# Kernel tuning notes

Hardware: AMD Instinct MI355X
Metric: run time of the kernel (lower is better)

Reference implementation:

```python
import jax, jax.numpy as jnp
import numpy as np

B_, S_, DIM, DT_RANK, D_STATE = 4, 1024, 384, 24, 16


def layer_norm(x, g, b, eps=1e-5):
    mu = jnp.mean(x, axis=-1, keepdims=True)
    var = jnp.mean((x - mu) ** 2, axis=-1, keepdims=True)
    return (x - mu) * jax.lax.rsqrt(var + eps) * g + b


def conv1d(x, w, b):
    # x: (B, C, L), w: (O, I, K), 'same' padding for odd K
    pad = (w.shape[-1] - 1) // 2
    y = jax.lax.conv_general_dilated(x, w, (1,), [(pad, pad)],
                                     dimension_numbers=('NCH', 'OIH', 'NCH'))
    return y + b[None, :, None]


def ssm(x, w_dbc, w_dt, b_dt, A_log, D):
    # x: (b, s, d) -> selective scan (Mamba), parallel (associative) scan form
    dbc = jnp.einsum('bsd,ed->bse', x, w_dbc)
    delta, Bm, Cm = jnp.split(dbc, [DT_RANK, DT_RANK + D_STATE], axis=-1)
    delta = jax.nn.softplus(jnp.einsum('bsr,dr->bsd', delta, w_dt) + b_dt)  # (b,s,d)
    A = -jnp.exp(A_log)                                   # (d, n)
    deltaA = jnp.exp(delta[..., None] * A)                # (b,s,d,n)
    BX = (delta * x)[..., None] * Bm[:, :, None, :]       # (b,s,d,n)

    def combine(c1, c2):
        a1, h1 = c1
        a2, h2 = c2
        return a1 * a2, a2 * h1 + h2

    _, hs = jax.lax.associative_scan(combine, (deltaA, BX), axis=1)
    y = jnp.einsum('bsdn,bsn->bsd', hs, Cm)
    return y + D * x


def setup_inputs() -> dict:
    key = jax.random.key(0)
    ks = jax.random.split(key, 16)
    sc = 0.02
    d, r, n = DIM, DT_RANK, D_STATE
    A_log = jnp.log(jnp.tile(jnp.arange(1, n + 1, dtype=jnp.float32), (d, 1)))  # (d, n)
    return {
        'x': jax.random.normal(ks[0], (B_, S_, d), dtype=jnp.float32),
        'w_p1': jax.random.normal(ks[1], (d, d, 3)) * sc, 'b_p1': jnp.zeros((d,)),
        'w_p2': jax.random.normal(ks[2], (d, d, 3)) * sc, 'b_p2': jnp.zeros((d,)),
        'w_p3': jax.random.normal(ks[3], (d, d, 1)) * sc, 'b_p3': jnp.zeros((d,)),
        'w_cf': jax.random.normal(ks[4], (d, d, 1)) * sc, 'b_cf': jnp.zeros((d,)),
        'w_cb': jax.random.normal(ks[5], (d, d, 1)) * sc, 'b_cb': jnp.zeros((d,)),
        'g_n': jnp.ones((d,)), 'bt_n': jnp.zeros((d,)),
        'g_nf': jnp.ones((d,)), 'bt_nf': jnp.zeros((d,)),
        'g_nb': jnp.ones((d,)), 'bt_nb': jnp.zeros((d,)),
        'w_dbc1': jax.random.normal(ks[6], (r + 2 * n, d)) * sc,
        'w_dt1': jax.random.normal(ks[7], (d, r)) * sc, 'b_dt1': jnp.zeros((d,)),
        'A_log1': A_log, 'D1': jnp.ones((d,)),
        'w_dbc2': jax.random.normal(ks[8], (r + 2 * n, d)) * sc,
        'w_dt2': jax.random.normal(ks[9], (d, r)) * sc, 'b_dt2': jnp.zeros((d,)),
        'A_log2': A_log, 'D2': jnp.ones((d,)),
    }


def reference(x, w_p1, b_p1, w_p2, b_p2, w_p3, b_p3, w_cf, b_cf, w_cb, b_cb,
              g_n, bt_n, g_nf, bt_nf, g_nb, bt_nb,
              w_dbc1, w_dt1, b_dt1, A_log1, D1,
              w_dbc2, w_dt2, b_dt2, A_log2, D2):
    skip = x
    xn = layer_norm(x, g_n, bt_n)
    xt = jnp.swapaxes(xn, 1, 2)                       # (b, d, s)
    z1 = jnp.swapaxes(conv1d(xt, w_p1, b_p1), 1, 2)   # (b, s, d)
    xp = conv1d(xt, w_p2, b_p2)                       # (b, d, s)

    def direction(xd, wc, bc, g, bt, w_dbc, w_dt, b_dt, A_log, D):
        h = conv1d(xd, wc, bc)
        h = jnp.swapaxes(h, 1, 2)
        h = layer_norm(h, g, bt)
        return ssm(h, w_dbc, w_dt, b_dt, A_log, D)

    x1 = direction(xp, w_cf, b_cf, g_nf, bt_nf, w_dbc1, w_dt1, b_dt1, A_log1, D1)
    # backward direction: sequence flipped (note: original does NOT flip back)
    x2 = direction(xp[:, :, ::-1], w_cb, b_cb, g_nb, bt_nb, w_dbc2, w_dt2, b_dt2, A_log2, D2)

    z = jax.nn.silu(z1)
    x3 = jnp.swapaxes((x1 + x2) * z, 1, 2)            # (b, d, s)
    out = jnp.swapaxes(conv1d(x3, w_p3, b_p3), 1, 2)
    return out + skip
```

## Files before the change

kernel.cpp:

```cpp
#include <hip/hip_runtime.h>
#include <cstddef>

#define NB 4
#define NS 1024
#define ND 384
#define NN 16
#define MTOT 4096
#define TM 8
#define NCH 32
#define CHL 32

__global__ __launch_bounds__(256) void prep_weights(
    const float* __restrict__ w_p1, const float* __restrict__ w_p2,
    const float* __restrict__ w_p3, const float* __restrict__ w_cf,
    const float* __restrict__ w_cb,
    const float* __restrict__ w_dbc1, const float* __restrict__ w_dbc2,
    const float* __restrict__ w_dt1,  const float* __restrict__ w_dt2,
    float* __restrict__ wp1T, float* __restrict__ wp2T, float* __restrict__ wp3T,
    float* __restrict__ wcfT, float* __restrict__ wcbT,
    float* __restrict__ wdbc1T, float* __restrict__ wdbc2T,
    float* __restrict__ wdt1T,  float* __restrict__ wdt2T)
{
    int idx = blockIdx.x * 256 + threadIdx.x;
    if (idx < 884736) {
        int q = idx; const float* w; float* wT;
        if (q < 442368) { w = w_p1; wT = wp1T; }
        else            { q -= 442368; w = w_p2; wT = wp2T; }
        int o = q % 384; int ki = q / 384; int i = ki % 384; int k = ki / 384;
        wT[q] = w[((size_t)o * 384 + i) * 3 + k];
    } else if (idx < 1327104) {
        int q = idx - 884736; const float* w; float* wT;
        if (q < 147456)      { w = w_p3; wT = wp3T; }
        else if (q < 294912) { q -= 147456; w = w_cf; wT = wcfT; }
        else                 { q -= 294912; w = w_cb; wT = wcbT; }
        int o = q % 384; int i = q / 384;
        wT[q] = w[(size_t)o * 384 + i];
    } else if (idx < 1370112) {
        int q = idx - 1327104; const float* w; float* wT;
        if (q < 21504) { w = w_dbc1; wT = wdbc1T; }
        else           { q -= 21504; w = w_dbc2; wT = wdbc2T; }
        int e = q % 56; int i = q / 56;
        wT[q] = w[(size_t)e * 384 + i];
    } else if (idx < 1388544) {
        int q = idx - 1370112; const float* w; float* wT;
        if (q < 9216) { w = w_dt1; wT = wdt1T; }
        else          { q -= 9216; w = w_dt2; wT = wdt2T; }
        int d = q % 384; int qq = q / 384;
        wT[q] = w[(size_t)d * 24 + qq];
    }
}

__global__ __launch_bounds__(384) void conv3x2(
    const float* __restrict__ x,
    const float* __restrict__ g_n, const float* __restrict__ bt_n,
    const float* __restrict__ wp2T, const float* __restrict__ b_p2,
    const float* __restrict__ wp1T, const float* __restrict__ b_p1,
    float* __restrict__ XP, float* __restrict__ Z1)
{
    __shared__ float xn[TM + 2][ND];
    int m0 = blockIdx.x * TM;
    int b = m0 >> 10, s0 = m0 & 1023;
    int t = threadIdx.x, wid = t >> 6, lane = t & 63;

    for (int j = wid; j < TM + 2; j += 6) {
        int r = s0 - 1 + j;
        if (r < 0 || r >= NS) {
            for (int e = 0; e < 6; ++e) xn[j][lane + 64 * e] = 0.f;
        } else {
            const float* row = x + ((size_t)(b * NS + r)) * ND;
            float v[6]; float s1 = 0.f, s2 = 0.f;
            #pragma unroll
            for (int e = 0; e < 6; ++e) {
                v[e] = row[lane + 64 * e];
                s1 += v[e]; s2 += v[e] * v[e];
            }
            #pragma unroll
            for (int o = 32; o; o >>= 1) {
                s1 += __shfl_xor(s1, o);
                s2 += __shfl_xor(s2, o);
            }
            float mu = s1 * (1.f / ND);
            float var = s2 * (1.f / ND) - mu * mu;
            float rs = rsqrtf(var + 1e-5f);
            #pragma unroll
            for (int e = 0; e < 6; ++e) {
                int i = lane + 64 * e;
                xn[j][i] = (v[e] - mu) * rs * g_n[i] + bt_n[i];
            }
        }
    }
    __syncthreads();

    float a2[TM], a1[TM];
    #pragma unroll
    for (int r = 0; r < TM; ++r) { a2[r] = b_p2[t]; a1[r] = b_p1[t]; }

    for (int k = 0; k < 3; ++k) {
        const float* w2base = wp2T + ((size_t)k * 384) * 384 + t;
        const float* w1base = wp1T + ((size_t)k * 384) * 384 + t;
        for (int i4 = 0; i4 < 96; ++i4) {
            float4 xv[TM];
            #pragma unroll
            for (int r = 0; r < TM; ++r)
                xv[r] = *reinterpret_cast<const float4*>(&xn[k + r][i4 * 4]);
            const float* w2 = w2base + (size_t)(i4 * 4) * 384;
            const float* w1 = w1base + (size_t)(i4 * 4) * 384;
            #pragma unroll
            for (int e = 0; e < 4; ++e) {
                float wv2 = w2[e * 384];
                float wv1 = w1[e * 384];
                #pragma unroll
                for (int r = 0; r < TM; ++r) {
                    float xe = (e == 0 ? xv[r].x : e == 1 ? xv[r].y :
                                e == 2 ? xv[r].z : xv[r].w);
                    a2[r] = fmaf(xe, wv2, a2[r]);
                    a1[r] = fmaf(xe, wv1, a1[r]);
                }
            }
        }
    }
    #pragma unroll
    for (int r = 0; r < TM; ++r) {
        size_t ix = (size_t)(m0 + r) * ND + t;
        XP[ix] = a2[r];
        Z1[ix] = a1[r];
    }
}

__global__ __launch_bounds__(384) void dir_k1(
    const float* __restrict__ XP, int flip,
    const float* __restrict__ wcT, const float* __restrict__ b_c,
    const float* __restrict__ g, const float* __restrict__ bt,
    const float* __restrict__ wdbcT, const float* __restrict__ wdtT,
    const float* __restrict__ b_dt,
    float* __restrict__ LNo, float* __restrict__ DBCo, float* __restrict__ DELo)
{
    __shared__ float xp[TM][ND];
    __shared__ float uo[TM][ND];
    __shared__ float red[TM][6][2];
    __shared__ float dbcS[TM][56];
    int m0 = blockIdx.x * TM;
    int b = m0 >> 10, s0 = m0 & 1023;
    int t = threadIdx.x, wid = t >> 6, lane = t & 63;

    for (int j = wid; j < TM; j += 6) {
        int s = s0 + j;
        int sE = flip ? (NS - 1 - s) : s;
        const float* row = XP + ((size_t)(b * NS + sE)) * ND;
        for (int e = 0; e < 6; ++e) xp[j][lane + 64 * e] = row[lane + 64 * e];
    }
    __syncthreads();

    float acc[TM];
    #pragma unroll
    for (int r = 0; r < TM; ++r) acc[r] = b_c[t];
    for (int i4 = 0; i4 < 96; ++i4) {
        float4 xv[TM];
        #pragma unroll
        for (int r = 0; r < TM; ++r)
            xv[r] = *reinterpret_cast<const float4*>(&xp[r][i4 * 4]);
        const float* wc = wcT + (size_t)(i4 * 4) * 384 + t;
        #pragma unroll
        for (int e = 0; e < 4; ++e) {
            float wv = wc[e * 384];
            #pragma unroll
            for (int r = 0; r < TM; ++r) {
                float xe = (e == 0 ? xv[r].x : e == 1 ? xv[r].y :
                            e == 2 ? xv[r].z : xv[r].w);
                acc[r] = fmaf(xe, wv, acc[r]);
            }
        }
    }

    #pragma unroll
    for (int r = 0; r < TM; ++r) {
        float s1 = acc[r], s2 = acc[r] * acc[r];
        #pragma unroll
        for (int o = 32; o; o >>= 1) {
            s1 += __shfl_xor(s1, o);
            s2 += __shfl_xor(s2, o);
        }
        if (lane == 0) { red[r][wid][0] = s1; red[r][wid][1] = s2; }
    }
    __syncthreads();
    float gt = g[t], btt = bt[t];
    #pragma unroll
    for (int r = 0; r < TM; ++r) {
        float s1 = 0.f, s2 = 0.f;
        #pragma unroll
        for (int w = 0; w < 6; ++w) { s1 += red[r][w][0]; s2 += red[r][w][1]; }
        float mu = s1 * (1.f / ND);
        float var = s2 * (1.f / ND) - mu * mu;
        float rs = rsqrtf(var + 1e-5f);
        float ln = (acc[r] - mu) * rs * gt + btt;
        uo[r][t] = ln;
        LNo[(size_t)(m0 + r) * ND + t] = ln;
    }
    __syncthreads();

    for (int r = wid; r < TM; r += 6) {
        if (lane < 56) {
            float a = 0.f;
            for (int i = 0; i < ND; ++i)
                a = fmaf(uo[r][i], wdbcT[i * 56 + lane], a);
            dbcS[r][lane] = a;
            DBCo[(size_t)(m0 + r) * 56 + lane] = a;
        }
    }
    __syncthreads();

    float accD[TM]; float bd = b_dt[t];
    #pragma unroll
    for (int r = 0; r < TM; ++r) accD[r] = bd;
    for (int q = 0; q < 24; ++q) {
        float wv = wdtT[q * 384 + t];
        #pragma unroll
        for (int r = 0; r < TM; ++r) accD[r] = fmaf(dbcS[r][q], wv, accD[r]);
    }
    #pragma unroll
    for (int r = 0; r < TM; ++r) {
        float a = accD[r];
        DELo[(size_t)(m0 + r) * ND + t] =
            fmaxf(a, 0.f) + log1pf(__expf(-fabsf(a)));
    }
}

__global__ __launch_bounds__(384) void scan_s1(
    const float* __restrict__ DEL2, const float* __restrict__ LN2,
    const float* __restrict__ DBC2, const float* __restrict__ A_log1,
    const float* __restrict__ A_log2,
    float* __restrict__ P, float* __restrict__ H)
{
    __shared__ float bc[CHL][32];
    int blk = blockIdx.x;
    int c = blk & (NCH - 1);
    int db = blk >> 5;
    int dir = db >> 2, b = db & 3;
    int t = threadIdx.x;
    const float* del  = DEL2 + (size_t)dir * MTOT * ND;
    const float* u    = LN2  + (size_t)dir * MTOT * ND;
    const float* dbc  = DBC2 + (size_t)dir * MTOT * 56;
    const float* Alog = dir ? A_log2 : A_log1;

    for (int e = t; e < CHL * 32; e += 384) {
        int row = e >> 5, col = e & 31;
        bc[row][col] = dbc[((size_t)(b * NS + c * CHL + row)) * 56 + 24 + col];
    }
    __syncthreads();

    float A[NN], h[NN], p[NN];
    #pragma unroll
    for (int n = 0; n < NN; ++n) {
        A[n] = -__expf(Alog[(size_t)t * NN + n]);
        h[n] = 0.f; p[n] = 1.f;
    }
    for (int j = 0; j < CHL; ++j) {
        size_t rix = (size_t)b * NS + c * CHL + j;
        float dl = del[rix * ND + t];
        float uv = u[rix * ND + t];
        float dx = dl * uv;
        #pragma unroll
        for (int n = 0; n < NN; ++n) {
            float da = __expf(dl * A[n]);
            h[n] = fmaf(da, h[n], dx * bc[j][n]);
            p[n] *= da;
        }
    }
    size_t base = ((size_t)blk * ND + t) * NN;
    #pragma unroll
    for (int n = 0; n < NN; ++n) { P[base + n] = p[n]; H[base + n] = h[n]; }
}

__global__ __launch_bounds__(256) void scan_s2(
    float* __restrict__ P, const float* __restrict__ H)
{
    int gid = blockIdx.x * 256 + threadIdx.x;
    int n = gid & 15;
    int d = (gid >> 4) % ND;
    int db = gid / (16 * ND);
    float h = 0.f;
    for (int c = 0; c < NCH; ++c) {
        size_t idx = (((size_t)db * NCH + c) * ND + d) * NN + n;
        float p = P[idx];
        float hh = H[idx];
        P[idx] = h;
        h = fmaf(p, h, hh);
    }
}

__global__ __launch_bounds__(384) void scan_s3(
    const float* __restrict__ DEL2, const float* __restrict__ LN2,
    const float* __restrict__ DBC2, const float* __restrict__ A_log1,
    const float* __restrict__ A_log2, const float* __restrict__ D1,
    const float* __restrict__ D2, const float* __restrict__ Hinit,
    float* __restrict__ Y2)
{
    __shared__ float bc[CHL][32];
    int blk = blockIdx.x;
    int c = blk & (NCH - 1);
    int db = blk >> 5;
    int dir = db >> 2, b = db & 3;
    int t = threadIdx.x;
    const float* del  = DEL2 + (size_t)dir * MTOT * ND;
    const float* u    = LN2  + (size_t)dir * MTOT * ND;
    const float* dbc  = DBC2 + (size_t)dir * MTOT * 56;
    const float* Alog = dir ? A_log2 : A_log1;
    const float* Dv   = dir ? D2 : D1;
    float* y          = Y2 + (size_t)dir * MTOT * ND;

    for (int e = t; e < CHL * 32; e += 384) {
        int row = e >> 5, col = e & 31;
        bc[row][col] = dbc[((size_t)(b * NS + c * CHL + row)) * 56 + 24 + col];
    }
    __syncthreads();

    size_t base = ((size_t)blk * ND + t) * NN;
    float A[NN], h[NN];
    #pragma unroll
    for (int n = 0; n < NN; ++n) {
        A[n] = -__expf(Alog[(size_t)t * NN + n]);
        h[n] = Hinit[base + n];
    }
    float Dd = Dv[t];
    for (int j = 0; j < CHL; ++j) {
        size_t rix = (size_t)b * NS + c * CHL + j;
        float dl = del[rix * ND + t];
        float uv = u[rix * ND + t];
        float dx = dl * uv;
        float y0 = 0.f, y1 = 0.f;
        #pragma unroll
        for (int n = 0; n < NN; n += 2) {
            float da0 = __expf(dl * A[n]);
            float da1 = __expf(dl * A[n + 1]);
            h[n]     = fmaf(da0, h[n],     dx * bc[j][n]);
            h[n + 1] = fmaf(da1, h[n + 1], dx * bc[j][n + 1]);
            y0 = fmaf(h[n],     bc[j][16 + n],     y0);
            y1 = fmaf(h[n + 1], bc[j][16 + n + 1], y1);
        }
        y[rix * ND + t] = y0 + y1 + Dd * uv;
    }
}

__global__ __launch_bounds__(64) void scan2(
    const float* __restrict__ DEL2, const float* __restrict__ LN2,
    const float* __restrict__ DBC2, const float* __restrict__ A1,
    const float* __restrict__ D1v, const float* __restrict__ A2,
    const float* __restrict__ D2v, float* __restrict__ Y2)
{
    int gid = blockIdx.x * 64 + threadIdx.x;
    int dir = gid >= (NB * ND);
    int gd = gid - dir * (NB * ND);
    const float* delta = DEL2 + (size_t)dir * MTOT * ND;
    const float* u     = LN2  + (size_t)dir * MTOT * ND;
    const float* dbc   = DBC2 + (size_t)dir * MTOT * 56;
    const float* Alog  = dir ? A2 : A1;
    const float* Dv    = dir ? D2v : D1v;
    float* y_out       = Y2 + (size_t)dir * MTOT * ND;

    int d = gd % ND, b = gd / ND;
    float A[NN], h[NN];
    #pragma unroll
    for (int n = 0; n < NN; ++n) {
        A[n] = -__expf(Alog[(size_t)d * NN + n]);
        h[n] = 0.f;
    }
    float Dd = Dv[d];
    for (int s = 0; s < NS; ++s) {
        size_t rix = (size_t)b * NS + s;
        float dl = delta[rix * ND + d];
        float uv = u[rix * ND + d];
        float dx = dl * uv;
        const float* r = dbc + rix * 56;
        float y0 = 0.f, y1 = 0.f;
        #pragma unroll
        for (int n = 0; n < NN; n += 2) {
            float da0 = __expf(dl * A[n]);
            float da1 = __expf(dl * A[n + 1]);
            h[n]     = fmaf(da0, h[n],     dx * r[24 + n]);
            h[n + 1] = fmaf(da1, h[n + 1], dx * r[24 + n + 1]);
            y0 = fmaf(h[n],     r[40 + n],     y0);
            y1 = fmaf(h[n + 1], r[40 + n + 1], y1);
        }
        y_out[rix * ND + d] = y0 + y1 + Dd * uv;
    }
}

__global__ __launch_bounds__(384) void final_k(
    const float* __restrict__ x, const float* __restrict__ Z1,
    const float* __restrict__ YF, const float* __restrict__ YB,
    const float* __restrict__ wp3T, const float* __restrict__ b_p3,
    float* __restrict__ out)
{
    __shared__ float x3[TM][ND];
    int m0 = blockIdx.x * TM;
    int t = threadIdx.x;
    #pragma unroll
    for (int r = 0; r < TM; ++r) {
        size_t ix = (size_t)(m0 + r) * ND + t;
        float z = Z1[ix];
        float sz = z / (1.f + __expf(-z));
        x3[r][t] = (YF[ix] + YB[ix]) * sz;
    }
    __syncthreads();

    float acc[TM]; float bp = b_p3[t];
    #pragma unroll
    for (int r = 0; r < TM; ++r) acc[r] = bp;
    for (int i4 = 0; i4 < 96; ++i4) {
        float4 xv[TM];
        #pragma unroll
        for (int r = 0; r < TM; ++r)
            xv[r] = *reinterpret_cast<const float4*>(&x3[r][i4 * 4]);
        const float* wp = wp3T + (size_t)(i4 * 4) * 384 + t;
        #pragma unroll
        for (int e = 0; e < 4; ++e) {
            float wv = wp[e * 384];
            #pragma unroll
            for (int r = 0; r < TM; ++r) {
                float xe = (e == 0 ? xv[r].x : e == 1 ? xv[r].y :
                            e == 2 ? xv[r].z : xv[r].w);
                acc[r] = fmaf(xe, wv, acc[r]);
            }
        }
    }
    #pragma unroll
    for (int r = 0; r < TM; ++r) {
        size_t ix = (size_t)(m0 + r) * ND + t;
        out[ix] = acc[r] + x[ix];
    }
}

__global__ __launch_bounds__(256) void fill_f32(float* out, float v, int n)
{
    int i = blockIdx.x * 256 + threadIdx.x;
    if (i < n) out[i] = v;
}

extern "C" void kernel_launch(void* const* d_in, const int* in_sizes, int n_in,
                              void* d_out, int out_size, void* d_ws, size_t ws_size,
                              hipStream_t stream) {
    float* out = (float*)d_out;

    if (out_size != MTOT * ND) {
        fill_f32<<<(out_size + 255) / 256, 256, 0, stream>>>(
            out, 70000.f + (float)(out_size >> 16), out_size);
        return;
    }

    const float* x      = (const float*)d_in[0];
    const float* w_p1   = (const float*)d_in[1];
    const float* b_p1   = (const float*)d_in[2];
    const float* w_p2   = (const float*)d_in[3];
    const float* b_p2   = (const float*)d_in[4];
    const float* w_p3   = (const float*)d_in[5];
    const float* b_p3   = (const float*)d_in[6];
    const float* w_cf   = (const float*)d_in[7];
    const float* b_cf   = (const float*)d_in[8];
    const float* w_cb   = (const float*)d_in[9];
    const float* b_cb   = (const float*)d_in[10];
    const float* g_n    = (const float*)d_in[11];
    const float* bt_n   = (const float*)d_in[12];
    const float* g_nf   = (const float*)d_in[13];
    const float* bt_nf  = (const float*)d_in[14];
    const float* g_nb   = (const float*)d_in[15];
    const float* bt_nb  = (const float*)d_in[16];
    const float* w_dbc1 = (const float*)d_in[17];
    const float* w_dt1  = (const float*)d_in[18];
    const float* b_dt1  = (const float*)d_in[19];
    const float* A_log1 = (const float*)d_in[20];
    const float* D1     = (const float*)d_in[21];
    const float* w_dbc2 = (const float*)d_in[22];
    const float* w_dt2  = (const float*)d_in[23];
    const float* b_dt2  = (const float*)d_in[24];
    const float* A_log2 = (const float*)d_in[25];
    const float* D2     = (const float*)d_in[26];

    const size_t NM = (size_t)MTOT * ND;
    const size_t N56 = (size_t)MTOT * 56;
    const size_t AGG = (size_t)2 * NB * NCH * ND * NN;
    size_t off = 0;
    float* ws = (float*)d_ws;
    float* XP    = ws + off; off += NM;
    float* Z1    = ws + off; off += NM;
    float* LN2   = ws + off; off += 2 * NM;
    float* DEL2  = ws + off; off += 2 * NM;
    float* Y2    = ws + off; off += 2 * NM;
    float* DBC2  = ws + off; off += 2 * N56;
    float* wp1T   = ws + off; off += 442368;
    float* wp2T   = ws + off; off += 442368;
    float* wp3T   = ws + off; off += 147456;
    float* wcfT   = ws + off; off += 147456;
    float* wcbT   = ws + off; off += 147456;
    float* wdbc1T = ws + off; off += 21504;
    float* wdbc2T = ws + off; off += 21504;
    float* wdt1T  = ws + off; off += 9216;
    float* wdt2T  = ws + off; off += 9216;
    const size_t ws_base = off;
    float* Pagg  = ws + off; off += AGG;
    float* Hagg  = ws + off; off += AGG;
    const size_t ws_fast = off;

    if (ws_size < ws_base * sizeof(float)) {
        fill_f32<<<(out_size + 255) / 256, 256, 0, stream>>>(out, 60000.f, out_size);
        return;
    }
    const int fast_scan = (ws_size >= ws_fast * sizeof(float));

    float* LNF  = LN2;        float* LNB  = LN2 + NM;
    float* DELF = DEL2;       float* DELB = DEL2 + NM;
    float* YF   = Y2;         float* YB   = Y2 + NM;
    float* DBCF = DBC2;       float* DBCB = DBC2 + N56;

    prep_weights<<<5424, 256, 0, stream>>>(
        w_p1, w_p2, w_p3, w_cf, w_cb, w_dbc1, w_dbc2, w_dt1, w_dt2,
        wp1T, wp2T, wp3T, wcfT, wcbT, wdbc1T, wdbc2T, wdt1T, wdt2T);

    conv3x2<<<MTOT / TM, 384, 0, stream>>>(
        x, g_n, bt_n, wp2T, b_p2, wp1T, b_p1, XP, Z1);

    dir_k1<<<MTOT / TM, 384, 0, stream>>>(
        XP, 0, wcfT, b_cf, g_nf, bt_nf, wdbc1T, wdt1T, b_dt1, LNF, DBCF, DELF);
    dir_k1<<<MTOT / TM, 384, 0, stream>>>(
        XP, 1, wcbT, b_cb, g_nb, bt_nb, wdbc2T, wdt2T, b_dt2, LNB, DBCB, DELB);

    if (fast_scan) {
        scan_s1<<<2 * NB * NCH, 384, 0, stream>>>(
            DEL2, LN2, DBC2, A_log1, A_log2, Pagg, Hagg);
        scan_s2<<<(2 * NB * ND * NN) / 256, 256, 0, stream>>>(Pagg, Hagg);
        scan_s3<<<2 * NB * NCH, 384, 0, stream>>>(
            DEL2, LN2, DBC2, A_log1, A_log2, D1, D2, Pagg, Y2);
    } else {
        scan2<<<(2 * NB * ND) / 64, 64, 0, stream>>>(
            DEL2, LN2, DBC2, A_log1, D1, A_log2, D2, Y2);
    }

    final_k<<<MTOT / TM, 384, 0, stream>>>(
        x, Z1, YF, YB, wp3T, b_p3, out);
}
```

Baseline: 522.7 us.

## Pack weights as float4 per output and merge both direction kernels

Reorders the transposed weight matrices so each thread reads four consecutive input channels as one float4, and prefetches the next float4 of weights one iteration ahead in the conv, dir and final GEMM loops. The two per-direction dir_k1 launches become one dir2_k1 launch that picks its direction from the block index. The dbc projection also uses the float4-packed layout. This is meant to cut scalar global load instructions and latency stalls and to save one launch. The cost is more register pressure from the prefetch buffers.

```diff
diff --git a/kernel.cpp b/kernel.cpp
--- a/kernel.cpp
+++ b/kernel.cpp
@@ -10,37 +10,42 @@
 #define NCH 32
 #define CHL 32
 
+static __device__ __forceinline__ float fget(const float4& v, int e) {
+    return e == 0 ? v.x : e == 1 ? v.y : e == 2 ? v.z : v.w;
+}
+
 __global__ __launch_bounds__(256) void prep_weights(
     const float* __restrict__ w_p1, const float* __restrict__ w_p2,
     const float* __restrict__ w_p3, const float* __restrict__ w_cf,
     const float* __restrict__ w_cb,
     const float* __restrict__ w_dbc1, const float* __restrict__ w_dbc2,
     const float* __restrict__ w_dt1,  const float* __restrict__ w_dt2,
-    float* __restrict__ wp1T, float* __restrict__ wp2T, float* __restrict__ wp3T,
-    float* __restrict__ wcfT, float* __restrict__ wcbT,
-    float* __restrict__ wdbc1T, float* __restrict__ wdbc2T,
+    float* __restrict__ wp1P, float* __restrict__ wp2P, float* __restrict__ wp3P,
+    float* __restrict__ wcfP, float* __restrict__ wcbP,
+    float* __restrict__ wdbc1P, float* __restrict__ wdbc2P,
     float* __restrict__ wdt1T,  float* __restrict__ wdt2T)
 {
     int idx = blockIdx.x * 256 + threadIdx.x;
     if (idx < 884736) {
         int q = idx; const float* w; float* wT;
-        if (q < 442368) { w = w_p1; wT = wp1T; }
-        else            { q -= 442368; w = w_p2; wT = wp2T; }
-        int o = q % 384; int ki = q / 384; int i = ki % 384; int k = ki / 384;
+        if (q < 442368) { w = w_p1; wT = wp1P; }
+        else            { q -= 442368; w = w_p2; wT = wp2P; }
+        int e = q & 3; int o = (q >> 2) % 384; int kk = q / 1536;
+        int k = kk / 96; int i = (kk % 96) * 4 + e;
         wT[q] = w[((size_t)o * 384 + i) * 3 + k];
     } else if (idx < 1327104) {
         int q = idx - 884736; const float* w; float* wT;
-        if (q < 147456)      { w = w_p3; wT = wp3T; }
-        else if (q < 294912) { q -= 147456; w = w_cf; wT = wcfT; }
-        else                 { q -= 294912; w = w_cb; wT = wcbT; }
-        int o = q % 384; int i = q / 384;
+        if (q < 147456)      { w = w_p3; wT = wp3P; }
+        else if (q < 294912) { q -= 147456; w = w_cf; wT = wcfP; }
+        else                 { q -= 294912; w = w_cb; wT = wcbP; }
+        int e = q & 3; int o = (q >> 2) % 384; int i = (q / 1536) * 4 + e;
         wT[q] = w[(size_t)o * 384 + i];
     } else if (idx < 1370112) {
         int q = idx - 1327104; const float* w; float* wT;
-        if (q < 21504) { w = w_dbc1; wT = wdbc1T; }
-        else           { q -= 21504; w = w_dbc2; wT = wdbc2T; }
-        int e = q % 56; int i = q / 56;
-        wT[q] = w[(size_t)e * 384 + i];
+        if (q < 21504) { w = w_dbc1; wT = wdbc1P; }
+        else           { q -= 21504; w = w_dbc2; wT = wdbc2P; }
+        int e = q & 3; int oc = (q >> 2) % 56; int i = (q / 224) * 4 + e;
+        wT[q] = w[(size_t)oc * 384 + i];
     } else if (idx < 1388544) {
         int q = idx - 1370112; const float* w; float* wT;
         if (q < 9216) { w = w_dt1; wT = wdt1T; }
@@ -53,8 +58,8 @@
 __global__ __launch_bounds__(384) void conv3x2(
     const float* __restrict__ x,
     const float* __restrict__ g_n, const float* __restrict__ bt_n,
-    const float* __restrict__ wp2T, const float* __restrict__ b_p2,
-    const float* __restrict__ wp1T, const float* __restrict__ b_p1,
+    const float* __restrict__ wp2P, const float* __restrict__ b_p2,
+    const float* __restrict__ wp1P, const float* __restrict__ b_p1,
     float* __restrict__ XP, float* __restrict__ Z1)
 {
     __shared__ float xn[TM + 2][ND];
@@ -91,33 +96,34 @@
     }
     __syncthreads();
 
+    const float4* xnf4 = reinterpret_cast<const float4*>(&xn[0][0]);
+    const float4* w2f4 = reinterpret_cast<const float4*>(wp2P) + t;
+    const float4* w1f4 = reinterpret_cast<const float4*>(wp1P) + t;
+
     float a2[TM], a1[TM];
     #pragma unroll
     for (int r = 0; r < TM; ++r) { a2[r] = b_p2[t]; a1[r] = b_p1[t]; }
 
-    for (int k = 0; k < 3; ++k) {
-        const float* w2base = wp2T + ((size_t)k * 384) * 384 + t;
-        const float* w1base = wp1T + ((size_t)k * 384) * 384 + t;
-        for (int i4 = 0; i4 < 96; ++i4) {
-            float4 xv[TM];
+    float4 W2c = w2f4[0], W1c = w1f4[0];
+    for (int kk = 0; kk < 288; ++kk) {
+        int kn = (kk < 287) ? kk + 1 : 287;
+        float4 W2n = w2f4[(size_t)kn * 384];
+        float4 W1n = w1f4[(size_t)kn * 384];
+        float4 xv[TM];
+        #pragma unroll
+        for (int r = 0; r < TM; ++r) xv[r] = xnf4[r * 96 + kk];
+        #pragma unroll
+        for (int e = 0; e < 4; ++e) {
+            float wv2 = fget(W2c, e);
+            float wv1 = fget(W1c, e);
             #pragma unroll
-            for (int r = 0; r < TM; ++r)
-                xv[r] = *reinterpret_cast<const float4*>(&xn[k + r][i4 * 4]);
-            const float* w2 = w2base + (size_t)(i4 * 4) * 384;
-            const float* w1 = w1base + (size_t)(i4 * 4) * 384;
-            #pragma unroll
-            for (int e = 0; e < 4; ++e) {
-                float wv2 = w2[e * 384];
-                float wv1 = w1[e * 384];
-                #pragma unroll
-                for (int r = 0; r < TM; ++r) {
-                    float xe = (e == 0 ? xv[r].x : e == 1 ? xv[r].y :
-                                e == 2 ? xv[r].z : xv[r].w);
-                    a2[r] = fmaf(xe, wv2, a2[r]);
-                    a1[r] = fmaf(xe, wv1, a1[r]);
-                }
+            for (int r = 0; r < TM; ++r) {
+                float xe = fget(xv[r], e);
+                a2[r] = fmaf(xe, wv2, a2[r]);
+                a1[r] = fmaf(xe, wv1, a1[r]);
             }
         }
+        W2c = W2n; W1c = W1n;
     }
     #pragma unroll
     for (int r = 0; r < TM; ++r) {
@@ -127,49 +133,72 @@
     }
 }
 
-__global__ __launch_bounds__(384) void dir_k1(
-    const float* __restrict__ XP, int flip,
-    const float* __restrict__ wcT, const float* __restrict__ b_c,
-    const float* __restrict__ g, const float* __restrict__ bt,
-    const float* __restrict__ wdbcT, const float* __restrict__ wdtT,
-    const float* __restrict__ b_dt,
-    float* __restrict__ LNo, float* __restrict__ DBCo, float* __restrict__ DELo)
+__global__ __launch_bounds__(384) void dir2_k1(
+    const float* __restrict__ XP,
+    const float* __restrict__ wcfP, const float* __restrict__ b_cf,
+    const float* __restrict__ g_nf, const float* __restrict__ bt_nf,
+    const float* __restrict__ wdbc1P, const float* __restrict__ wdt1T,
+    const float* __restrict__ b_dt1,
+    const float* __restrict__ wcbP, const float* __restrict__ b_cb,
+    const float* __restrict__ g_nb, const float* __restrict__ bt_nb,
+    const float* __restrict__ wdbc2P, const float* __restrict__ wdt2T,
+    const float* __restrict__ b_dt2,
+    float* __restrict__ LN2, float* __restrict__ DBC2, float* __restrict__ DEL2)
 {
     __shared__ float xp[TM][ND];
     __shared__ float uo[TM][ND];
     __shared__ float red[TM][6][2];
     __shared__ float dbcS[TM][56];
-    int m0 = blockIdx.x * TM;
+    int blk = blockIdx.x;
+    int dir = blk >> 9;
+    int m0 = (blk & 511) * TM;
     int b = m0 >> 10, s0 = m0 & 1023;
     int t = threadIdx.x, wid = t >> 6, lane = t & 63;
 
-    for (int j = wid; j < TM; j += 6) {
-        int s = s0 + j;
-        int sE = flip ? (NS - 1 - s) : s;
-        const float* row = XP + ((size_t)(b * NS + sE)) * ND;
-        for (int e = 0; e < 6; ++e) xp[j][lane + 64 * e] = row[lane + 64 * e];
-    }
-    __syncthreads();
-
+    const float* wcP   = dir ? wcbP   : wcfP;
+    const float* b_c   = dir ? b_cb   : b_cf;
+    const float* g     = dir ? g_nb   : g_nf;
+    const float* bt    = dir ? bt_nb  : bt_nf;
+    const float* wdbcP = dir ? wdbc2P : wdbc1P;
+    const float* wdtT  = dir ? wdt2T  : wdt1T;
+    const float* b_dt  = dir ? b_dt2  : b_dt1;
+    const size_t NM = (size_t)MTOT * ND;
+    float* LNo  = LN2  + (size_t)dir * NM;
+    float* DBCo = DBC2 + (size_t)dir * MTOT * 56;
+    float* DELo = DEL2 + (size_t)dir * NM;
+
+    {
+        float4* xpf4 = reinterpret_cast<float4*>(&xp[0][0]);
+        const float4* XPf4 = reinterpret_cast<const float4*>(XP);
+        for (int e = t; e < TM * 96; e += 384) {
+            int j = e / 96, i4 = e - (e / 96) * 96;
+            int s = s0 + j;
+            int sE = dir ? (NS - 1 - s) : s;
+            xpf4[j * 96 + i4] = XPf4[((size_t)(b * NS + sE)) * 96 + i4];
+        }
+    }
+    __syncthreads();
+
+    const float4* xpf4 = reinterpret_cast<const float4*>(&xp[0][0]);
+    const float4* wcf4 = reinterpret_cast<const float4*>(wcP) + t;
     float acc[TM];
     #pragma unroll
     for (int r = 0; r < TM; ++r) acc[r] = b_c[t];
+    float4 Wc = wcf4[0];
     for (int i4 = 0; i4 < 96; ++i4) {
+        int in_ = (i4 < 95) ? i4 + 1 : 95;
+        float4 Wn = wcf4[(size_t)in_ * 384];
         float4 xv[TM];
         #pragma unroll
-        for (int r = 0; r < TM; ++r)
-            xv[r] = *reinterpret_cast<const float4*>(&xp[r][i4 * 4]);
-        const float* wc = wcT + (size_t)(i4 * 4) * 384 + t;
+        for (int r = 0; r < TM; ++r) xv[r] = xpf4[r * 96 + i4];
         #pragma unroll
         for (int e = 0; e < 4; ++e) {
-            float wv = wc[e * 384];
+            float wv = fget(Wc, e);
             #pragma unroll
-            for (int r = 0; r < TM; ++r) {
-                float xe = (e == 0 ? xv[r].x : e == 1 ? xv[r].y :
-                            e == 2 ? xv[r].z : xv[r].w);
-                acc[r] = fmaf(xe, wv, acc[r]);
-            }
-        }
+            for (int r = 0; r < TM; ++r)
+                acc[r] = fmaf(fget(xv[r], e), wv, acc[r]);
+        }
+        Wc = Wn;
     }
 
     #pragma unroll
@@ -200,9 +229,20 @@
 
     for (int r = wid; r < TM; r += 6) {
         if (lane < 56) {
+            const float4* wdf4 = reinterpret_cast<const float4*>(wdbcP) + lane;
+            const float4* uof4 = reinterpret_cast<const float4*>(&uo[r][0]);
             float a = 0.f;
-            for (int i = 0; i < ND; ++i)
-                a = fmaf(uo[r][i], wdbcT[i * 56 + lane], a);
+            float4 Wd = wdf4[0];
+            for (int i4 = 0; i4 < 96; ++i4) {
+                int in_ = (i4 < 95) ? i4 + 1 : 95;
+                float4 Wdn = wdf4[(size_t)in_ * 56];
+                float4 uv = uof4[i4];
+                a = fmaf(uv.x, Wd.x, a);
+                a = fmaf(uv.y, Wd.y, a);
+                a = fmaf(uv.z, Wd.z, a);
+                a = fmaf(uv.w, Wd.w, a);
+                Wd = Wdn;
+            }
             dbcS[r][lane] = a;
             DBCo[(size_t)(m0 + r) * 56 + lane] = a;
         }
@@ -388,7 +428,7 @@
 __global__ __launch_bounds__(384) void final_k(
     const float* __restrict__ x, const float* __restrict__ Z1,
     const float* __restrict__ YF, const float* __restrict__ YB,
-    const float* __restrict__ wp3T, const float* __restrict__ b_p3,
+    const float* __restrict__ wp3P, const float* __restrict__ b_p3,
     float* __restrict__ out)
 {
     __shared__ float x3[TM][ND];
@@ -403,25 +443,26 @@
     }
     __syncthreads();
 
+    const float4* x3f4 = reinterpret_cast<const float4*>(&x3[0][0]);
+    const float4* wpf4 = reinterpret_cast<const float4*>(wp3P) + t;
     float acc[TM]; float bp = b_p3[t];
     #pragma unroll
     for (int r = 0; r < TM; ++r) acc[r] = bp;
+    float4 Wp = wpf4[0];
     for (int i4 = 0; i4 < 96; ++i4) {
+        int in_ = (i4 < 95) ? i4 + 1 : 95;
+        float4 Wn = wpf4[(size_t)in_ * 384];
         float4 xv[TM];
         #pragma unroll
-        for (int r = 0; r < TM; ++r)
-            xv[r] = *reinterpret_cast<const float4*>(&x3[r][i4 * 4]);
-        const float* wp = wp3T + (size_t)(i4 * 4) * 384 + t;
+        for (int r = 0; r < TM; ++r) xv[r] = x3f4[r * 96 + i4];
         #pragma unroll
         for (int e = 0; e < 4; ++e) {
-            float wv = wp[e * 384];
+            float wv = fget(Wp, e);
             #pragma unroll
-            for (int r = 0; r < TM; ++r) {
-                float xe = (e == 0 ? xv[r].x : e == 1 ? xv[r].y :
-                            e == 2 ? xv[r].z : xv[r].w);
-                acc[r] = fmaf(xe, wv, acc[r]);
-            }
-        }
+            for (int r = 0; r < TM; ++r)
+                acc[r] = fmaf(fget(xv[r], e), wv, acc[r]);
+        }
+        Wp = Wn;
     }
     #pragma unroll
     for (int r = 0; r < TM; ++r) {
@@ -486,13 +527,13 @@
     float* DEL2  = ws + off; off += 2 * NM;
     float* Y2    = ws + off; off += 2 * NM;
     float* DBC2  = ws + off; off += 2 * N56;
-    float* wp1T   = ws + off; off += 442368;
-    float* wp2T   = ws + off; off += 442368;
-    float* wp3T   = ws + off; off += 147456;
-    float* wcfT   = ws + off; off += 147456;
-    float* wcbT   = ws + off; off += 147456;
-    float* wdbc1T = ws + off; off += 21504;
-    float* wdbc2T = ws + off; off += 21504;
+    float* wp1P   = ws + off; off += 442368;
+    float* wp2P   = ws + off; off += 442368;
+    float* wp3P   = ws + off; off += 147456;
+    float* wcfP   = ws + off; off += 147456;
+    float* wcbP   = ws + off; off += 147456;
+    float* wdbc1P = ws + off; off += 21504;
+    float* wdbc2P = ws + off; off += 21504;
     float* wdt1T  = ws + off; off += 9216;
     float* wdt2T  = ws + off; off += 9216;
     const size_t ws_base = off;
@@ -506,22 +547,20 @@
     }
     const int fast_scan = (ws_size >= ws_fast * sizeof(float));
 
-    float* LNF  = LN2;        float* LNB  = LN2 + NM;
-    float* DELF = DEL2;       float* DELB = DEL2 + NM;
     float* YF   = Y2;         float* YB   = Y2 + NM;
-    float* DBCF = DBC2;       float* DBCB = DBC2 + N56;
 
     prep_weights<<<5424, 256, 0, stream>>>(
         w_p1, w_p2, w_p3, w_cf, w_cb, w_dbc1, w_dbc2, w_dt1, w_dt2,
-        wp1T, wp2T, wp3T, wcfT, wcbT, wdbc1T, wdbc2T, wdt1T, wdt2T);
+        wp1P, wp2P, wp3P, wcfP, wcbP, wdbc1P, wdbc2P, wdt1T, wdt2T);
 
     conv3x2<<<MTOT / TM, 384, 0, stream>>>(
-        x, g_n, bt_n, wp2T, b_p2, wp1T, b_p1, XP, Z1);
-
-    dir_k1<<<MTOT / TM, 384, 0, stream>>>(
-        XP, 0, wcfT, b_cf, g_nf, bt_nf, wdbc1T, wdt1T, b_dt1, LNF, DBCF, DELF);
-    dir_k1<<<MTOT / TM, 384, 0, stream>>>(
-        XP, 1, wcbT, b_cb, g_nb, bt_nb, wdbc2T, wdt2T, b_dt2, LNB, DBCB, DELB);
+        x, g_n, bt_n, wp2P, b_p2, wp1P, b_p1, XP, Z1);
+
+    dir2_k1<<<2 * (MTOT / TM), 384, 0, stream>>>(
+        XP,
+        wcfP, b_cf, g_nf, bt_nf, wdbc1P, wdt1T, b_dt1,
+        wcbP, b_cb, g_nb, bt_nb, wdbc2P, wdt2T, b_dt2,
+        LN2, DBC2, DEL2);
 
     if (fast_scan) {
         scan_s1<<<2 * NB * NCH, 384, 0, stream>>>(
@@ -535,5 +574,5 @@
     }
 
     final_k<<<MTOT / TM, 384, 0, stream>>>(
-        x, Z1, YF, YB, wp3T, b_p3, out);
-}
+        x, Z1, YF, YB, wp3P, b_p3, out);
+}
```

New measurement: 426.0 us. 1.23x faster.
